# Kernel optimization log

Measured on AMD Instinct MI355X. Metric: run time of the kernel, lower is better.

## Reference

```python
import jax, jax.numpy as jnp
import numpy as np

# norse LIFParameters / LIParameters defaults
DT = 1e-3
TAU_SYN_INV = 200.0   # 1/5e-3
TAU_MEM_INV = 100.0   # 1/1e-2
V_TH = 1.0
V_LEAK = 0.0
V_RESET = 0.0
ALPHA = 100.0         # super-spike surrogate slope
SEQ = 10              # ConstantCurrentLIFEncoder(10)
SCALE = 50.0

@jax.custom_vjp
def superspike(x):
    # forward: Heaviside; backward: SuperSpike surrogate 1/(alpha|x|+1)^2
    return (x > 0).astype(x.dtype)

def _ss_fwd(x):
    return superspike(x), x

def _ss_bwd(x, g):
    return (g / (ALPHA * jnp.abs(x) + 1.0) ** 2,)

superspike.defvjp(_ss_fwd, _ss_bwd)

def constant_current_lif_encode(current):
    # current: (B, S) constant input current; returns spikes (SEQ, B, S)
    def step(v, _):
        v = v + DT * TAU_MEM_INV * ((V_LEAK - v) + current)
        z = superspike(v - V_TH)
        v = v - z * (v - V_RESET)
        return v, z
    _, spikes = jax.lax.scan(step, jnp.zeros_like(current), None, length=SEQ)
    return spikes

def setup_inputs() -> dict:
    key = jax.random.key(0)
    k1, k2, k3, k4 = jax.random.split(key, 4)
    B, S, H, A = 2048, 2048, 256, 16
    x = jax.random.normal(k1, (B, S), dtype=jnp.float32)
    w_in = jax.random.normal(k2, (H, 2 * S), dtype=jnp.float32) * np.float32(np.sqrt(2.0 / H))
    w_rec = jax.random.normal(k3, (H, H), dtype=jnp.float32) * np.float32(np.sqrt(2.0 / H))
    w_rec = w_rec * (1.0 - jnp.eye(H, dtype=jnp.float32))  # no autapses
    w_out = jax.random.normal(k4, (A, H), dtype=jnp.float32) * np.float32(np.sqrt(2.0 / H))
    return {"x": x, "w_in": w_in, "w_rec": w_rec, "w_out": w_out}

def reference(x, w_in, w_rec, w_out):
    # PPOSNN.pi(x): encode, LIF recurrent scan, LI readout, max over time, softmax
    enc = jnp.concatenate(
        [constant_current_lif_encode(jax.nn.relu(SCALE * x)),
         constant_current_lif_encode(jax.nn.relu(-SCALE * x))],
        axis=2,
    )  # (SEQ, B, 2S)
    B = x.shape[0]
    H = w_rec.shape[0]
    A = w_out.shape[0]
    z0 = jnp.zeros((B, H), x.dtype)
    v0 = jnp.zeros((B, H), x.dtype)
    i0 = jnp.zeros((B, H), x.dtype)
    vo0 = jnp.zeros((B, A), x.dtype)
    io0 = jnp.zeros((B, A), x.dtype)

    def step(carry, inp):
        z, v, i, vo, io = carry
        # LIFRecurrentCell (norse lif_step)
        v_dec = v + DT * TAU_MEM_INV * ((V_LEAK - v) + i)
        i_dec = i * (1.0 - DT * TAU_SYN_INV)
        z_new = superspike(v_dec - V_TH)
        v_new = (1.0 - z_new) * v_dec + z_new * V_RESET
        i_new = i_dec + inp @ w_in.T + z @ w_rec.T
        # LILinearCell (norse li_step) on z_new
        vo_new = vo + DT * TAU_MEM_INV * ((V_LEAK - vo) + io)
        io_new = io * (1.0 - DT * TAU_SYN_INV) + z_new @ w_out.T
        return (z_new, v_new, i_new, vo_new, io_new), vo_new

    _, voltages = jax.lax.scan(step, (z0, v0, i0, vo0, io0), enc)  # (SEQ, B, A)
    m = jnp.max(voltages, axis=0)
    m = jnp.where(jnp.isnan(m), jnp.zeros_like(m), m)
    return jax.nn.softmax(m, axis=1)
```

## Files before the change

kernel.cpp:

```cpp
#include <hip/hip_runtime.h>
#include <stdint.h>
#include <stddef.h>

typedef __attribute__((ext_vector_type(8))) short short8;
typedef __attribute__((ext_vector_type(4))) float f32x4;
typedef __attribute__((ext_vector_type(16))) float f32x16;
typedef __attribute__((ext_vector_type(4))) uint32_t u32x4;

#define GLD_LDS16(gsrc, ldst)                                                   \
    __builtin_amdgcn_global_load_lds(                                           \
        (const __attribute__((address_space(1))) uint32_t*)(const void*)(gsrc), \
        (__attribute__((address_space(3))) uint32_t*)(void*)(ldst), 16, 0, 0)

static __device__ __forceinline__ uint16_t bf16_rne(float f) {
    uint32_t u = __float_as_uint(f);
    uint32_t r = u + 0x7FFFu + ((u >> 16) & 1u);
    return (uint16_t)(r >> 16);
}
static __device__ __forceinline__ float bf16_f(uint16_t h) {
    return __uint_as_float(((uint32_t)h) << 16);
}

#define OFF_MASKS 0u
#define SZ_MASKS  (2048u * 4096u * 2u)
#define OFF_WIN   (OFF_MASKS + SZ_MASKS)
#define SZ_WIN1   (256u * 4096u * 2u)
#define OFF_WREC  (OFF_WIN + 3u * SZ_WIN1)
#define SZ_WREC1  (256u * 256u * 2u)
#define OFF_WOUT  (OFF_WREC + 2u * SZ_WREC1)
#define SZ_WOUT1  (16u * 256u * 2u)
#define OFF_IIN   (OFF_WOUT + 2u * SZ_WOUT1)

__global__ __launch_bounds__(256) void k_prep(const float* __restrict__ x,
                                              uint16_t* __restrict__ masks) {
    int g = blockIdx.x * 256 + threadIdx.x;
    int b = g >> 11, s = g & 2047;
    float q = 50.0f * x[g];
    float c = fabsf(q);
    float v = 0.0f;
    uint32_t m = 0u;
    #pragma unroll
    for (int t = 0; t < 10; ++t) {
        v = v + 0.1f * ((0.0f - v) + c);
        if (v > 1.0f) { m |= (1u << t); v = 0.0f; }
    }
    masks[(size_t)b * 4096 + s]        = (q > 0.0f) ? (uint16_t)m : (uint16_t)0;
    masks[(size_t)b * 4096 + 2048 + s] = (q < 0.0f) ? (uint16_t)m : (uint16_t)0;
}

__global__ __launch_bounds__(256) void k_wsplit(const float* __restrict__ win,
                                                const float* __restrict__ wrec,
                                                const float* __restrict__ wout,
                                                uint16_t* __restrict__ win_s,
                                                uint16_t* __restrict__ wrec_s,
                                                uint16_t* __restrict__ wout_s) {
    int g = blockIdx.x * 256 + threadIdx.x;
    if (g < 1048576) {
        float w = win[g];
        uint16_t h = bf16_rne(w);
        float r1 = w - bf16_f(h);
        uint16_t md = bf16_rne(r1);
        float r2 = r1 - bf16_f(md);
        win_s[g]            = h;
        win_s[1048576 + g]  = md;
        win_s[2097152 + g]  = bf16_rne(r2);
    } else if (g < 1114112) {
        int i = g - 1048576;
        float w = wrec[i];
        uint16_t h = bf16_rne(w);
        float r1 = w - bf16_f(h);
        wrec_s[i]         = h;
        wrec_s[65536 + i] = bf16_rne(r1);
    } else if (g < 1118208) {
        int i = g - 1114112;
        float w = wout[i];
        uint16_t h = bf16_rne(w);
        float r1 = w - bf16_f(h);
        wout_s[i]        = h;
        wout_s[4096 + i] = bf16_rne(r1);
    }
}

__global__ __launch_bounds__(256, 3) void k_gemm(const uint16_t* __restrict__ masks,
                                                 const uint16_t* __restrict__ wsp,
                                                 float* __restrict__ iin) {
    __shared__ uint16_t Bbuf[3][128 * 64];
    const int tid = threadIdx.x;
    const int lane = tid & 63;
    const int wid = tid >> 6;
    const int l31 = lane & 31;
    const int hi  = lane >> 5;
    const int Mtile = blockIdx.x >> 1;
    const int Ntile = blockIdx.x & 1;
    const int M0 = Mtile * 64;

    uint32_t bb[2], tt[2];
    #pragma unroll
    for (int mf = 0; mf < 2; ++mf) {
        uint32_t m = (uint32_t)(M0 + mf * 32 + l31);
        uint32_t b = (m * 52429u) >> 19;
        bb[mf] = b;
        tt[mf] = m - b * 10u;
    }

    u32x4 mq[2][4];
    auto loadMasks = [&](int kk) {
        #pragma unroll
        for (int mf = 0; mf < 2; ++mf) {
            const uint16_t* mp = masks + (size_t)bb[mf] * 4096 + (size_t)(kk * 64 + hi * 8);
            #pragma unroll
            for (int ks = 0; ks < 4; ++ks)
                mq[mf][ks] = *(const u32x4*)(mp + ks * 16);
        }
    };

    short8 af[2][4];
    auto expand = [&]() {
        #pragma unroll
        for (int mf = 0; mf < 2; ++mf)
            #pragma unroll
            for (int ks = 0; ks < 4; ++ks) {
                u32x4 o;
                #pragma unroll
                for (int w = 0; w < 4; ++w) {
                    uint32_t x = mq[mf][ks][w] >> tt[mf];
                    o[w] = (x & 0x10001u) * 0x3F80u;
                }
                af[mf][ks] = *(short8*)&o;
            }
    };

    auto stageB = [&](int kk, int s, uint16_t* bufp) {
        const char* src = (const char*)wsp + (size_t)s * 2097152u;
        char* dst = (char*)bufp;
        #pragma unroll
        for (int p = 0; p < 4; ++p) {
            int c = (p << 8) + tid;
            int n = c >> 3;
            uint32_t off = (uint32_t)((c & 7) << 4);
            uint32_t so = (uint32_t)(Ntile * 128 + n) * 8192u + (uint32_t)(kk << 7)
                        + (off ^ (uint32_t)((n & 7) << 4));
            GLD_LDS16(src + so, dst + (size_t)c * 16u);
        }
    };

    f32x16 acc[2];
    #pragma unroll
    for (int mf = 0; mf < 2; ++mf)
        #pragma unroll
        for (int q = 0; q < 16; ++q) acc[mf][q] = 0.0f;

    auto mfmaPhase = [&](const uint16_t* Bp) {
        short8 bf[4];
        const int n = (wid << 5) + l31;
        #pragma unroll
        for (int ks = 0; ks < 4; ++ks) {
            uint32_t byte = (uint32_t)(n * 128)
                          + ((uint32_t)((ks << 5) + (hi << 4)) ^ (uint32_t)((n & 7) << 4));
            bf[ks] = *(const short8*)((const char*)Bp + byte);
        }
        __builtin_amdgcn_s_setprio(1);
        #pragma unroll
        for (int ks = 0; ks < 4; ++ks)
            #pragma unroll
            for (int mf = 0; mf < 2; ++mf)
                acc[mf] = __builtin_amdgcn_mfma_f32_32x32x16_bf16(
                    af[mf][ks], bf[ks], acc[mf], 0, 0, 0);
        __builtin_amdgcn_s_setprio(0);
    };

    loadMasks(0);
    stageB(0, 0, Bbuf[0]);
    asm volatile("s_waitcnt vmcnt(4)" ::: "memory");
    expand();

    #pragma unroll 1
    for (int kk = 0; kk < 64; ++kk) {
        const bool more = (kk < 63);
        stageB(kk, 1, Bbuf[1]);
        asm volatile("s_waitcnt vmcnt(4)" ::: "memory");
        __builtin_amdgcn_s_barrier();
        __builtin_amdgcn_sched_barrier(0);
        mfmaPhase(Bbuf[0]);
        stageB(kk, 2, Bbuf[2]);
        if (more) {
            loadMasks(kk + 1);
            asm volatile("s_waitcnt vmcnt(12)" ::: "memory");
        } else {
            asm volatile("s_waitcnt vmcnt(4)" ::: "memory");
        }
        __builtin_amdgcn_s_barrier();
        __builtin_amdgcn_sched_barrier(0);
        mfmaPhase(Bbuf[1]);
        if (more) {
            stageB(kk + 1, 0, Bbuf[0]);
            asm volatile("s_waitcnt vmcnt(4)" ::: "memory");
        } else {
            asm volatile("s_waitcnt vmcnt(0)" ::: "memory");
        }
        __builtin_amdgcn_s_barrier();
        __builtin_amdgcn_sched_barrier(0);
        mfmaPhase(Bbuf[2]);
        if (more) expand();
    }

    #pragma unroll
    for (int mf = 0; mf < 2; ++mf)
        #pragma unroll
        for (int r = 0; r < 16; ++r) {
            int row = (r & 3) + ((r >> 2) << 3) + (hi << 2);
            int gm = M0 + mf * 32 + row;
            int h = Ntile * 128 + (wid << 5) + l31;
            iin[(size_t)gm * 256 + h] = acc[mf][r];
        }
}

__global__ __launch_bounds__(256) void k_scan(const float* __restrict__ iin,
                                              const uint16_t* __restrict__ wrec_s,
                                              const uint16_t* __restrict__ wout_s,
                                              float* __restrict__ out) {
    __shared__ uint16_t Bb[2][256 * 128];
    __shared__ uint16_t Zb[16 * 256];
    __shared__ uint16_t WO[2][16 * 256];
    const int tid = threadIdx.x;
    const int lane = tid & 63;
    const int wid = tid >> 6;
    const int l15 = lane & 15;
    const int lq = lane >> 4;
    const int b0 = blockIdx.x << 3;

    auto stageBrec = [&](int g, int db) {
        int sp = (g >> 1) & 1;
        int kh = g & 1;
        const char* src = (const char*)wrec_s + (size_t)sp * 131072u;
        char* dst = (char*)Bb[db];
        #pragma unroll
        for (int p = 0; p < 16; ++p) {
            int c = (p << 8) + tid;
            int n = c >> 4;
            uint32_t x0 = (uint32_t)((c & 15) << 4);
            uint32_t so = (uint32_t)(n * 512) + (uint32_t)(kh << 8)
                        + (x0 ^ (uint32_t)((n & 7) << 4));
            GLD_LDS16(src + so, dst + (size_t)c * 16);
        }
    };

    stageBrec(0, 0);

    #pragma unroll
    for (int s = 0; s < 2; ++s) {
        #pragma unroll
        for (int p = 0; p < 2; ++p) {
            int c = (p << 8) + tid;
            int n = c >> 5;
            uint32_t off = (uint32_t)((c & 31) << 4);
            u32x4 v = *(const u32x4*)((const char*)(wout_s + (size_t)s * 4096) + (size_t)n * 512 + off);
            *(u32x4*)((char*)WO[s] + (uint32_t)(n * 512) + (off ^ (uint32_t)((n & 7) << 4))) = v;
        }
    }
    #pragma unroll
    for (int p = 0; p < 8; ++p) ((uint32_t*)Zb)[(p << 8) + tid] = 0u;

    asm volatile("s_waitcnt lgkmcnt(0)" ::: "memory");
    __builtin_amdgcn_s_barrier();

    float vst[4][4], ist[4][4];
    #pragma unroll
    for (int nf = 0; nf < 4; ++nf)
        #pragma unroll
        for (int r = 0; r < 4; ++r) { vst[nf][r] = 0.0f; ist[nf][r] = 0.0f; }
    float io_[4] = {0.f, 0.f, 0.f, 0.f};
    float vo_[4] = {0.f, 0.f, 0.f, 0.f};
    float mm[4] = {-1e30f, -1e30f, -1e30f, -1e30f};

    #pragma unroll 1
    for (int t = 0; t < 10; ++t) {
        f32x4 acc[4];
        uint32_t zb[4];
        #pragma unroll
        for (int nf = 0; nf < 4; ++nf) {
            zb[nf] = 0u;
            #pragma unroll
            for (int r = 0; r < 4; ++r) {
                int brow = (lq << 2) + r;
                float vv = vst[nf][r];
                float ii = ist[nf][r];
                float vd = vv + 0.1f * ((0.0f - vv) + ii);
                bool z = (vd > 1.0f);
                vst[nf][r] = z ? 0.0f : vd;
                if (z) zb[nf] |= (1u << r);
                int h = (wid << 6) + (nf << 4) + l15;
                int rowc = brow < 8 ? brow : 7;
                float I = iin[(size_t)((b0 + rowc) * 10 + t) * 256 + h];
                I = (brow < 8) ? I : 0.0f;
                acc[nf][r] = 0.8f * ii + I;
            }
        }
        for (int j = 0; j < 4; ++j) {
            int g = (t << 2) + j;
            int kh = g & 1;
            __builtin_amdgcn_s_barrier();
            if (g + 1 < 40) {
                stageBrec(g + 1, (g + 1) & 1);
                asm volatile("s_waitcnt vmcnt(16)" ::: "memory");
            } else {
                asm volatile("s_waitcnt vmcnt(0)" ::: "memory");
            }
            __builtin_amdgcn_s_barrier();
            __builtin_amdgcn_sched_barrier(0);
            short8 az[4];
            #pragma unroll
            for (int kt = 0; kt < 4; ++kt) {
                uint32_t byte = (uint32_t)(l15 * 512)
                              + ((uint32_t)((kh << 8) + (kt << 6) + (lq << 4))
                                 ^ (uint32_t)((l15 & 7) << 4));
                az[kt] = *(const short8*)((const char*)Zb + byte);
            }
            const char* Bp = (const char*)Bb[g & 1];
            __builtin_amdgcn_s_setprio(1);
            #pragma unroll
            for (int nf = 0; nf < 4; ++nf) {
                int n = (wid << 6) + (nf << 4) + l15;
                #pragma unroll
                for (int kt = 0; kt < 4; ++kt) {
                    uint32_t byte = (uint32_t)(n * 256)
                                  + ((uint32_t)((kt << 6) + (lq << 4)) ^ (uint32_t)((n & 7) << 4));
                    short8 bw = *(const short8*)(Bp + byte);
                    acc[nf] = __builtin_amdgcn_mfma_f32_16x16x32_bf16(az[kt], bw, acc[nf], 0, 0, 0);
                }
            }
            __builtin_amdgcn_s_setprio(0);
        }
        #pragma unroll
        for (int nf = 0; nf < 4; ++nf)
            #pragma unroll
            for (int r = 0; r < 4; ++r) ist[nf][r] = acc[nf][r];

        __builtin_amdgcn_s_barrier();
        #pragma unroll
        for (int nf = 0; nf < 4; ++nf)
            #pragma unroll
            for (int r = 0; r < 4; ++r) {
                int brow = (lq << 2) + r;
                if (brow < 8) {
                    int h = (wid << 6) + (nf << 4) + l15;
                    uint32_t byte = (uint32_t)(brow * 512)
                                  + ((uint32_t)(h << 1) ^ (uint32_t)((brow & 7) << 4));
                    *(uint16_t*)((char*)Zb + byte) =
                        ((zb[nf] >> r) & 1u) ? (uint16_t)0x3F80u : (uint16_t)0u;
                }
            }
        asm volatile("s_waitcnt lgkmcnt(0)" ::: "memory");
        __builtin_amdgcn_s_barrier();

        if (wid == 0) {
            f32x4 aio;
            #pragma unroll
            for (int r = 0; r < 4; ++r) aio[r] = 0.8f * io_[r];
            #pragma unroll
            for (int s = 0; s < 2; ++s) {
                #pragma unroll
                for (int kc = 0; kc < 8; ++kc) {
                    int kb = (kc << 6) + (lq << 4);
                    uint32_t byte = (uint32_t)(l15 * 512)
                                  + ((uint32_t)kb ^ (uint32_t)((l15 & 7) << 4));
                    short8 azn = *(const short8*)((const char*)Zb + byte);
                    short8 bwo = *(const short8*)((const char*)WO[s] + byte);
                    aio = __builtin_amdgcn_mfma_f32_16x16x32_bf16(azn, bwo, aio, 0, 0, 0);
                }
            }
            #pragma unroll
            for (int r = 0; r < 4; ++r) {
                float von = vo_[r] + 0.1f * ((0.0f - vo_[r]) + io_[r]);
                io_[r] = aio[r];
                vo_[r] = von;
                mm[r] = fmaxf(mm[r], von);
            }
        }
    }

    if (wid == 0 && lq < 2) {
        #pragma unroll
        for (int r = 0; r < 4; ++r) {
            float mv = mm[r];
            if (mv != mv) mv = 0.0f;
            float mx = mv;
            #pragma unroll
            for (int d = 1; d < 16; d <<= 1) mx = fmaxf(mx, __shfl_xor(mx, d));
            float e = __expf(mv - mx);
            float ss = e;
            #pragma unroll
            for (int d = 1; d < 16; d <<= 1) ss += __shfl_xor(ss, d);
            out[(size_t)(b0 + (lq << 2) + r) * 16 + l15] = e / ss;
        }
    }
}

extern "C" void kernel_launch(void* const* d_in, const int* in_sizes, int n_in,
                              void* d_out, int out_size, void* d_ws, size_t ws_size,
                              hipStream_t stream) {
    (void)in_sizes; (void)n_in; (void)out_size; (void)ws_size;
    const float* x     = (const float*)d_in[0];
    const float* w_in  = (const float*)d_in[1];
    const float* w_rec = (const float*)d_in[2];
    const float* w_out = (const float*)d_in[3];
    float* out = (float*)d_out;
    char* ws = (char*)d_ws;
    uint16_t* masks  = (uint16_t*)(ws + OFF_MASKS);
    uint16_t* win_s  = (uint16_t*)(ws + OFF_WIN);
    uint16_t* wrec_s = (uint16_t*)(ws + OFF_WREC);
    uint16_t* wout_s = (uint16_t*)(ws + OFF_WOUT);
    float* iin = (float*)(ws + OFF_IIN);

    k_prep  <<<dim3(16384), dim3(256), 0, stream>>>(x, masks);
    k_wsplit<<<dim3(4368),  dim3(256), 0, stream>>>(w_in, w_rec, w_out, win_s, wrec_s, wout_s);
    k_gemm  <<<dim3(640),   dim3(256), 0, stream>>>(masks, win_s, iin);
    k_scan  <<<dim3(256),   dim3(256), 0, stream>>>(iin, wrec_s, wout_s, out);
}
```

Before: 303.4 us.

## Retile input GEMM to 80-row M tiles using 16x16x32 MFMA

The input-current GEMM moves from 32x32x16 MFMA with 64-row M tiles to 16x16x32 MFMA with 80-row M tiles (5x2 fragments per wave). This cuts the grid from 640 to 512 blocks, so each staged B tile is reused across more rows and the block count fits the CU count more evenly. The cost is more accumulator registers and more mask loads per thread, and the occupancy hint of 3 blocks per CU is dropped.

```diff
diff --git a/kernel.cpp b/kernel.cpp
--- a/kernel.cpp
+++ b/kernel.cpp
@@ -4,7 +4,6 @@
 
 typedef __attribute__((ext_vector_type(8))) short short8;
 typedef __attribute__((ext_vector_type(4))) float f32x4;
-typedef __attribute__((ext_vector_type(16))) float f32x16;
 typedef __attribute__((ext_vector_type(4))) uint32_t u32x4;
 
 #define GLD_LDS16(gsrc, ldst)                                                   \
@@ -81,52 +80,51 @@
     }
 }
 
-__global__ __launch_bounds__(256, 3) void k_gemm(const uint16_t* __restrict__ masks,
-                                                 const uint16_t* __restrict__ wsp,
-                                                 float* __restrict__ iin) {
+__global__ __launch_bounds__(256) void k_gemm(const uint16_t* __restrict__ masks,
+                                              const uint16_t* __restrict__ wsp,
+                                              float* __restrict__ iin) {
     __shared__ uint16_t Bbuf[3][128 * 64];
     const int tid = threadIdx.x;
     const int lane = tid & 63;
     const int wid = tid >> 6;
-    const int l31 = lane & 31;
-    const int hi  = lane >> 5;
+    const int l15 = lane & 15;
+    const int lq = lane >> 4;
     const int Mtile = blockIdx.x >> 1;
     const int Ntile = blockIdx.x & 1;
-    const int M0 = Mtile * 64;
-
-    uint32_t bb[2], tt[2];
-    #pragma unroll
-    for (int mf = 0; mf < 2; ++mf) {
-        uint32_t m = (uint32_t)(M0 + mf * 32 + l31);
+    const int M0 = Mtile * 80;
+
+    uint32_t bb[5], tt[5];
+    #pragma unroll
+    for (int mt = 0; mt < 5; ++mt) {
+        uint32_t m = (uint32_t)(M0 + mt * 16 + l15);
         uint32_t b = (m * 52429u) >> 19;
-        bb[mf] = b;
-        tt[mf] = m - b * 10u;
-    }
-
-    u32x4 mq[2][4];
+        bb[mt] = b;
+        tt[mt] = m - b * 10u;
+    }
+
+    u32x4 mq[5][2];
     auto loadMasks = [&](int kk) {
         #pragma unroll
-        for (int mf = 0; mf < 2; ++mf) {
-            const uint16_t* mp = masks + (size_t)bb[mf] * 4096 + (size_t)(kk * 64 + hi * 8);
-            #pragma unroll
-            for (int ks = 0; ks < 4; ++ks)
-                mq[mf][ks] = *(const u32x4*)(mp + ks * 16);
-        }
+        for (int mt = 0; mt < 5; ++mt)
+            #pragma unroll
+            for (int kt = 0; kt < 2; ++kt)
+                mq[mt][kt] = *(const u32x4*)(masks + (size_t)bb[mt] * 4096
+                                             + (size_t)(kk * 64 + kt * 32 + lq * 8));
     };
 
-    short8 af[2][4];
+    short8 af[5][2];
     auto expand = [&]() {
         #pragma unroll
-        for (int mf = 0; mf < 2; ++mf)
-            #pragma unroll
-            for (int ks = 0; ks < 4; ++ks) {
+        for (int mt = 0; mt < 5; ++mt)
+            #pragma unroll
+            for (int kt = 0; kt < 2; ++kt) {
                 u32x4 o;
                 #pragma unroll
                 for (int w = 0; w < 4; ++w) {
-                    uint32_t x = mq[mf][ks][w] >> tt[mf];
+                    uint32_t x = mq[mt][kt][w] >> tt[mt];
                     o[w] = (x & 0x10001u) * 0x3F80u;
                 }
-                af[mf][ks] = *(short8*)&o;
+                af[mt][kt] = *(short8*)&o;
             }
     };
 
@@ -144,28 +142,34 @@
         }
     };
 
-    f32x16 acc[2];
-    #pragma unroll
-    for (int mf = 0; mf < 2; ++mf)
-        #pragma unroll
-        for (int q = 0; q < 16; ++q) acc[mf][q] = 0.0f;
-
-    auto mfmaPhase = [&](const uint16_t* Bp) {
-        short8 bf[4];
-        const int n = (wid << 5) + l31;
-        #pragma unroll
-        for (int ks = 0; ks < 4; ++ks) {
-            uint32_t byte = (uint32_t)(n * 128)
-                          + ((uint32_t)((ks << 5) + (hi << 4)) ^ (uint32_t)((n & 7) << 4));
-            bf[ks] = *(const short8*)((const char*)Bp + byte);
-        }
+    f32x4 acc[5][2];
+    #pragma unroll
+    for (int mt = 0; mt < 5; ++mt)
+        #pragma unroll
+        for (int nt = 0; nt < 2; ++nt)
+            #pragma unroll
+            for (int q = 0; q < 4; ++q) acc[mt][nt][q] = 0.0f;
+
+    auto mfmaPhase = [&](const uint16_t* Bpp) {
+        short8 bf[2][2];
+        #pragma unroll
+        for (int nt = 0; nt < 2; ++nt)
+            #pragma unroll
+            for (int kt = 0; kt < 2; ++kt) {
+                int n = (wid << 5) + nt * 16 + l15;
+                uint32_t byte = (uint32_t)(n * 128)
+                              + ((uint32_t)((kt << 6) + (lq << 4)) ^ (uint32_t)((n & 7) << 4));
+                bf[nt][kt] = *(const short8*)((const char*)Bpp + byte);
+            }
         __builtin_amdgcn_s_setprio(1);
         #pragma unroll
-        for (int ks = 0; ks < 4; ++ks)
-            #pragma unroll
-            for (int mf = 0; mf < 2; ++mf)
-                acc[mf] = __builtin_amdgcn_mfma_f32_32x32x16_bf16(
-                    af[mf][ks], bf[ks], acc[mf], 0, 0, 0);
+        for (int kt = 0; kt < 2; ++kt)
+            #pragma unroll
+            for (int mt = 0; mt < 5; ++mt)
+                #pragma unroll
+                for (int nt = 0; nt < 2; ++nt)
+                    acc[mt][nt] = __builtin_amdgcn_mfma_f32_16x16x32_bf16(
+                        af[mt][kt], bf[nt][kt], acc[mt][nt], 0, 0, 0);
         __builtin_amdgcn_s_setprio(0);
     };
 
@@ -185,7 +189,7 @@
         stageB(kk, 2, Bbuf[2]);
         if (more) {
             loadMasks(kk + 1);
-            asm volatile("s_waitcnt vmcnt(12)" ::: "memory");
+            asm volatile("s_waitcnt vmcnt(14)" ::: "memory");
         } else {
             asm volatile("s_waitcnt vmcnt(4)" ::: "memory");
         }
@@ -205,14 +209,15 @@
     }
 
     #pragma unroll
-    for (int mf = 0; mf < 2; ++mf)
-        #pragma unroll
-        for (int r = 0; r < 16; ++r) {
-            int row = (r & 3) + ((r >> 2) << 3) + (hi << 2);
-            int gm = M0 + mf * 32 + row;
-            int h = Ntile * 128 + (wid << 5) + l31;
-            iin[(size_t)gm * 256 + h] = acc[mf][r];
-        }
+    for (int mt = 0; mt < 5; ++mt)
+        #pragma unroll
+        for (int nt = 0; nt < 2; ++nt)
+            #pragma unroll
+            for (int i = 0; i < 4; ++i) {
+                int gm = M0 + mt * 16 + (lq << 2) + i;
+                int h = Ntile * 128 + (wid << 5) + nt * 16 + l15;
+                iin[(size_t)gm * 256 + h] = acc[mt][nt][i];
+            }
 }
 
 __global__ __launch_bounds__(256) void k_scan(const float* __restrict__ iin,
@@ -414,6 +419,6 @@
 
     k_prep  <<<dim3(16384), dim3(256), 0, stream>>>(x, masks);
     k_wsplit<<<dim3(4368),  dim3(256), 0, stream>>>(w_in, w_rec, w_out, win_s, wrec_s, wout_s);
-    k_gemm  <<<dim3(640),   dim3(256), 0, stream>>>(masks, win_s, iin);
+    k_gemm  <<<dim3(512),   dim3(256), 0, stream>>>(masks, win_s, iin);
     k_scan  <<<dim3(256),   dim3(256), 0, stream>>>(iin, wrec_s, wout_s, out);
 }
```

Result: faster. 259.7 us (-14.4%).
